# Kernel tuning notes

Measured on AMD Instinct MI355X. Metric: run time of the kernel, lower is better.

The kernel has to match this reference:

```python
import jax, jax.numpy as jnp
import numpy as np

NUM_CLASSES = 1203
C = NUM_CLASSES + 1
ITER = 9001            # > warm_up_iter=8000 (full path), not a multiple of save_iter=1000
GAMMA = 1.0
BETA = 1.0             # forward default loss_type=1 -> beta = 1
EMA = 0.999
LOWER = 1.0 / 3.0
UPPER = 5.0
LOSS_WEIGHT_ARG = 1.0  # forward `loss_weight` arg default
SELF_LOSS_WEIGHT = 1.0 # __init__ loss_weight
N = 16384              # multiple of 64 (interval in collect_grad_optim)


def setup_inputs() -> dict:
    key = jax.random.key(0)
    k1, k2, k3, k4, k5 = jax.random.split(key, 5)
    cls_score = jax.random.normal(k1, (N, C), jnp.float32)
    label = jax.random.randint(k2, (N,), 0, C)
    weight = jax.random.uniform(k3, (N,), jnp.float32)
    classes_logits = jax.random.normal(k4, (C,), jnp.float32) * 0.01
    class_weights_buf = jnp.ones((C,), jnp.float32)
    corr_grad_accu = jax.random.normal(k5, (C, C), jnp.float32) * 0.01
    weights_mean = jnp.ones((1,), jnp.float32)
    return {"cls_score": cls_score, "label": label, "weight": weight,
            "classes_logits": classes_logits, "class_weights_buf": class_weights_buf,
            "corr_grad_accu": corr_grad_accu, "weights_mean": weights_mean}


def reference(cls_score, label, weight, classes_logits, class_weights_buf,
              corr_grad_accu, weights_mean):
    sg = jax.lax.stop_gradient
    n = cls_score.shape[0]
    target = jax.nn.one_hot(label, C, dtype=cls_score.dtype)  # expand_label

    # ---- get_weight (no_grad in torch): beta=1, iter % save_iter != 0 ----
    cw = jnp.clip(class_weights_buf, LOWER, UPPER)
    tmp_weight = (cw ** BETA)[label]                 # (class_weights**beta * target).sum(1)
    wm = EMA * weights_mean[0] + (1.0 - EMA) * tmp_weight.mean()
    tmp_weight = tmp_weight / wm
    tmp_weight = sg(tmp_weight * weight)             # detached in torch

    # ---- focal cross-entropy ----
    logp = jax.nn.log_softmax(cls_score, axis=-1)
    CE = -jnp.take_along_axis(logp, label[:, None], axis=1)[:, 0]
    p = jnp.exp(-CE)
    loss = (1.0 - p) ** GAMMA * CE
    loss = (loss * tmp_weight).mean()                # weight_reduce_loss mean

    # ---- collect_grad_optim (all under no_grad in torch) ----
    cs = sg(cls_score)
    w = sg(weight)
    prob = jax.nn.softmax(cs, axis=-1) + 1e-5                       # [N,C]
    focal_grad = w[:, None] * ((1.0 - prob) / prob - jnp.log(prob)) # [N,C]
    pos_grad = ((1.0 - prob) * prob * focal_grad * target).mean(0)  # [C]
    # corr[i,j] = mean_n target[n,i]*focal_grad[n,i]*prob[n,i]*prob[n,j]
    a = target * focal_grad * prob                                  # [N,C]
    corr = jnp.einsum('ni,nj->ij', a, prob) / n                     # [C,C]
    diag = jnp.arange(C)
    corr = corr.at[diag, diag].set(-pos_grad)
    corr_grad = corr * 100.0 * LOSS_WEIGHT_ARG      # dist.all_reduce = identity (1 proc)

    # ITER >= warm_up_iter branch: EMA update + class weights from logits
    accu = EMA * sg(corr_grad_accu) + (1.0 - EMA) * corr_grad
    cw2 = sg(jax.nn.softmax(classes_logits)) * C    # detached in torch

    tcw = (cw2[:, None] * accu).sum(0) / (-jnp.diagonal(accu) + 1e-6) + cw2
    # ITER > warm_up_iter branch:
    tcw = tcw.at[-1].set(C - tcw[:-1].sum())
    tcw = jnp.clip(tcw, LOWER, UPPER)
    tcw = tcw.at[-1].set(jnp.clip(tcw[-1], LOWER, 1.0))
    tcw = sg(jnp.log(tcw))
    loss_grad = ((tcw - classes_logits) ** 2).mean()

    return (SELF_LOSS_WEIGHT * loss, loss_grad, cw2)
```

## Files before the change

### kernel.cpp

```cpp
#include <hip/hip_runtime.h>
#include <math.h>

#define C_   1204
#define C4_  301
#define NROWBLK 2048
#define BCAP 64
#define NYCHUNK 16
#define YLEN 76

__device__ __forceinline__ float waveReduceSum(float v){
    #pragma unroll
    for (int o = 32; o > 0; o >>= 1) v += __shfl_xor(v, o, 64);
    return v;
}
__device__ __forceinline__ float exp4(float4 v){
    return __expf(v.x) + __expf(v.y) + __expf(v.z) + __expf(v.w);
}
__device__ __forceinline__ float4 accExp(float4 acc, float sc, float4 x){
    acc.x += sc * __expf(x.x); acc.y += sc * __expf(x.y);
    acc.z += sc * __expf(x.z); acc.w += sc * __expf(x.w);
    return acc;
}

__global__ void k_pre(int* cursor, const float* __restrict__ logits,
                      float* cw2, float* out){
    int t = threadIdx.x;
    if (blockIdx.x > 0){
        int j = (blockIdx.x - 1) * 256 + t;
        if (j < C_) cursor[j] = 0;
        return;
    }
    __shared__ float red[256];
    float x[5]; float m = -3.402823466e38f;
    #pragma unroll
    for (int k = 0; k < 5; ++k){
        int j = t + k * 256;
        x[k] = (j < C_) ? logits[j] : -3.402823466e38f;
        m = fmaxf(m, x[k]);
    }
    red[t] = m; __syncthreads();
    for (int o = 128; o > 0; o >>= 1){ if (t < o) red[t] = fmaxf(red[t], red[t+o]); __syncthreads(); }
    float bm = red[0]; __syncthreads();
    float ss = 0.f;
    #pragma unroll
    for (int k = 0; k < 5; ++k){ int j = t + k * 256; if (j < C_) ss += __expf(x[k] - bm); }
    red[t] = ss; __syncthreads();
    for (int o = 128; o > 0; o >>= 1){ if (t < o) red[t] += red[t+o]; __syncthreads(); }
    float bs = red[0]; __syncthreads();
    #pragma unroll
    for (int k = 0; k < 5; ++k){
        int j = t + k * 256;
        if (j < C_){ float v = __expf(x[k] - bm) / bs * (float)C_; cw2[j] = v; out[2 + j] = v; }
    }
}

__global__ void k_rows(const float* __restrict__ cs, const int* __restrict__ label,
                       const float* __restrict__ w, const float* __restrict__ cwb,
                       float* __restrict__ rowsum, float* __restrict__ aN,
                       float* __restrict__ pN, int* cursor, int* bucket2,
                       float* __restrict__ part1, float* __restrict__ part2){
    int lane = threadIdx.x & 63;
    int wid  = threadIdx.x >> 6;
    int nA = (blockIdx.x * 4 + wid) * 2;
    int nB = nA + 1;
    const float4* rowA = reinterpret_cast<const float4*>(cs + (size_t)nA * C_);
    const float4* rowB = reinterpret_cast<const float4*>(cs + (size_t)nB * C_);
    bool has4 = lane < (C4_ - 256);

    float4 a0 = rowA[lane], a1 = rowA[lane + 64], a2 = rowA[lane + 128], a3 = rowA[lane + 192];
    float4 b0 = rowB[lane], b1 = rowB[lane + 64], b2 = rowB[lane + 128], b3 = rowB[lane + 192];
    float4 a4, b4;
    if (has4){ a4 = rowA[lane + 256]; b4 = rowB[lane + 256]; }

    float sA = exp4(a0) + exp4(a1) + exp4(a2) + exp4(a3);
    float sB = exp4(b0) + exp4(b1) + exp4(b2) + exp4(b3);
    if (has4){ sA += exp4(a4); sB += exp4(b4); }
    sA = waveReduceSum(sA);
    sB = waveReduceSum(sB);

    __shared__ float lr1[8], lr2[8];
    if (lane < 2){
        int   n = (lane == 0) ? nA : nB;
        float s = (lane == 0) ? sA : sB;
        rowsum[n] = s;
        int l = label[n];
        float x = cs[(size_t)n * C_ + l];
        float logp = x - __logf(s);
        float p = __expf(logp);
        float lossc = (1.f - p) * (-logp);
        float t = fminf(fmaxf(cwb[l], 1.f/3.f), 5.f);
        float wn = w[n];
        float pp = p + 1e-5f;
        float fg = wn * ((1.f - pp) / pp - __logf(pp));
        aN[n] = fg * pp;
        pN[n] = pp;
        int slot = atomicAdd(&cursor[l], 1);
        bucket2[l * BCAP + slot] = n;
        lr1[wid * 2 + lane] = lossc * t * wn;
        lr2[wid * 2 + lane] = t;
    }
    __syncthreads();
    if (threadIdx.x == 0){
        float s1 = 0.f, s2 = 0.f;
        #pragma unroll
        for (int k = 0; k < 8; ++k){ s1 += lr1[k]; s2 += lr2[k]; }
        part1[blockIdx.x] = s1;
        part2[blockIdx.x] = s2;
    }
}

__global__ void k_corr(const float* __restrict__ cs, const int* __restrict__ bucket2,
                       const int* __restrict__ cursor,
                       const float* __restrict__ rowsum, const float* __restrict__ aN,
                       const float* __restrict__ pN, const float* __restrict__ cga,
                       float* __restrict__ accu, float* __restrict__ diag, int Nn){
    int i = blockIdx.x;
    int t = threadIdx.x;
    int cnt = cursor[i];
    const int* bkt = bucket2 + i * BCAP;
    bool has2 = t < (C4_ - 256);
    float4 acc0 = {0.f,0.f,0.f,0.f}, acc1 = {0.f,0.f,0.f,0.f};
    float suma = 0.f, sumb = 0.f;

    int nbat = (cnt + 7) >> 3;
    for (int b = 0; b < nbat; ++b){
        int s = b << 3;
        #define LOADR(k) \
            int  id##k = min(s + k, cnt - 1); \
            int  n##k  = bkt[id##k]; \
            float va##k = aN[n##k]; \
            float pb##k = pN[n##k]; \
            float iv##k = (s + k < cnt) ? va##k / rowsum[n##k] : 0.f; \
            float ma##k = (s + k < cnt) ? va##k : 0.f; \
            const float4* rp##k = reinterpret_cast<const float4*>(cs + (size_t)n##k * C_); \
            float4 x0##k = rp##k[t]; \
            float4 x1##k; if (has2) x1##k = rp##k[t + 256];
        LOADR(0) LOADR(1) LOADR(2) LOADR(3) LOADR(4) LOADR(5) LOADR(6) LOADR(7)
        #undef LOADR
        suma += ma0 + ma1 + ma2 + ma3 + ma4 + ma5 + ma6 + ma7;
        sumb += ma0*pb0 + ma1*pb1 + ma2*pb2 + ma3*pb3
              + ma4*pb4 + ma5*pb5 + ma6*pb6 + ma7*pb7;
        acc0 = accExp(acc0, iv0, x00); acc0 = accExp(acc0, iv1, x01);
        acc0 = accExp(acc0, iv2, x02); acc0 = accExp(acc0, iv3, x03);
        acc0 = accExp(acc0, iv4, x04); acc0 = accExp(acc0, iv5, x05);
        acc0 = accExp(acc0, iv6, x06); acc0 = accExp(acc0, iv7, x07);
        if (has2){
            acc1 = accExp(acc1, iv0, x10); acc1 = accExp(acc1, iv1, x11);
            acc1 = accExp(acc1, iv2, x12); acc1 = accExp(acc1, iv3, x13);
            acc1 = accExp(acc1, iv4, x14); acc1 = accExp(acc1, iv5, x15);
            acc1 = accExp(acc1, iv6, x16); acc1 = accExp(acc1, iv7, x17);
        }
    }

    float eps   = suma * 1e-5f;
    float scale = 100.f / (float)Nn;
    float diagv = -100.f * (suma - sumb) / (float)Nn;
    const float4* cga4 = reinterpret_cast<const float4*>(cga + (size_t)i * C_);
    float4*       out4 = reinterpret_cast<float4*>(accu + (size_t)i * C_);
    int d4 = i >> 2, dc = i & 3;

    float4 cgv;
    cgv.x = (acc0.x + eps) * scale; cgv.y = (acc0.y + eps) * scale;
    cgv.z = (acc0.z + eps) * scale; cgv.w = (acc0.w + eps) * scale;
    if (t == d4){
        if (dc == 0) cgv.x = diagv; else if (dc == 1) cgv.y = diagv;
        else if (dc == 2) cgv.z = diagv; else cgv.w = diagv;
    }
    float4 gv = cga4[t];
    float4 wv;
    wv.x = 0.999f*gv.x + 0.001f*cgv.x; wv.y = 0.999f*gv.y + 0.001f*cgv.y;
    wv.z = 0.999f*gv.z + 0.001f*cgv.z; wv.w = 0.999f*gv.w + 0.001f*cgv.w;
    out4[t] = wv;
    if (t == d4)
        diag[i] = (dc == 0) ? wv.x : (dc == 1) ? wv.y : (dc == 2) ? wv.z : wv.w;

    if (has2){
        int t2 = t + 256;
        float4 cgv1;
        cgv1.x = (acc1.x + eps) * scale; cgv1.y = (acc1.y + eps) * scale;
        cgv1.z = (acc1.z + eps) * scale; cgv1.w = (acc1.w + eps) * scale;
        if (t2 == d4){
            if (dc == 0) cgv1.x = diagv; else if (dc == 1) cgv1.y = diagv;
            else if (dc == 2) cgv1.z = diagv; else cgv1.w = diagv;
        }
        float4 gv1 = cga4[t2];
        float4 wv1;
        wv1.x = 0.999f*gv1.x + 0.001f*cgv1.x; wv1.y = 0.999f*gv1.y + 0.001f*cgv1.y;
        wv1.z = 0.999f*gv1.z + 0.001f*cgv1.z; wv1.w = 0.999f*gv1.w + 0.001f*cgv1.w;
        out4[t2] = wv1;
        if (t2 == d4)
            diag[i] = (dc == 0) ? wv1.x : (dc == 1) ? wv1.y : (dc == 2) ? wv1.z : wv1.w;
    }
}

__global__ void k_matvec(const float* __restrict__ cw2, const float* __restrict__ accu,
                         float* __restrict__ tpart){
    int j = blockIdx.x * 256 + threadIdx.x;
    if (j >= C_) return;
    int i0 = blockIdx.y * YLEN, i1 = min(i0 + YLEN, C_);
    float p = 0.f;
    #pragma unroll 4
    for (int i = i0; i < i1; ++i) p += cw2[i] * accu[(size_t)i * C_ + j];
    tpart[blockIdx.y * C_ + j] = p;
}

__global__ void k_final(const float* __restrict__ tpart, const float* __restrict__ diag,
                        const float* __restrict__ cw2, const float* __restrict__ logits,
                        const float* __restrict__ part1, const float* __restrict__ part2,
                        const float* __restrict__ wm0, float* out, int Nn){
    __shared__ float tcw[C_];
    __shared__ float red[256];
    __shared__ float red2[256];
    int t = threadIdx.x;

    float p1 = 0.f, p2 = 0.f;
    for (int k = t; k < NROWBLK; k += 256){ p1 += part1[k]; p2 += part2[k]; }
    red[t] = p1; red2[t] = p2; __syncthreads();
    for (int o = 128; o > 0; o >>= 1){
        if (t < o){ red[t] += red[t+o]; red2[t] += red2[t+o]; }
        __syncthreads();
    }
    float sumLoss = red[0], sumT = red2[0];
    __syncthreads();

    float psum = 0.f;
    #pragma unroll
    for (int k = 0; k < 5; ++k){
        int j = t + k * 256;
        if (j < C_ - 1){
            float tc = 0.f;
            #pragma unroll
            for (int y = 0; y < NYCHUNK; ++y) tc += tpart[y * C_ + j];
            float denom = -diag[j] + 1e-6f;
            float v = tc / denom + cw2[j];
            tcw[j] = v; psum += v;
        }
    }
    red[t] = psum; __syncthreads();
    for (int o = 128; o > 0; o >>= 1){ if (t < o) red[t] += red[t+o]; __syncthreads(); }
    if (t == 0) tcw[C_ - 1] = (float)C_ - red[0];
    __syncthreads();
    float sq = 0.f;
    #pragma unroll
    for (int k = 0; k < 5; ++k){
        int j = t + k * 256;
        if (j < C_){
            float hi = (j == C_ - 1) ? 1.f : 5.f;
            float v = fminf(fmaxf(tcw[j], 1.f/3.f), hi);
            float d = logf(v) - logits[j];
            sq += d * d;
        }
    }
    red[t] = sq; __syncthreads();
    for (int o = 128; o > 0; o >>= 1){ if (t < o) red[t] += red[t+o]; __syncthreads(); }
    if (t == 0){
        float wm = 0.999f * wm0[0] + 0.001f * (sumT / (float)Nn);
        out[0] = sumLoss / ((float)Nn * wm);
        out[1] = red[0] / (float)C_;
    }
}

extern "C" void kernel_launch(void* const* d_in, const int* in_sizes, int n_in,
                              void* d_out, int out_size, void* d_ws, size_t ws_size,
                              hipStream_t stream){
    (void)n_in; (void)out_size; (void)ws_size;
    const float* cs     = (const float*)d_in[0];
    const int*   label  = (const int*)  d_in[1];
    const float* weight = (const float*)d_in[2];
    const float* logits = (const float*)d_in[3];
    const float* cwb    = (const float*)d_in[4];
    const float* cga    = (const float*)d_in[5];
    const float* wm0    = (const float*)d_in[6];
    float* out = (float*)d_out;
    const int N = in_sizes[1];

    float* ws      = (float*)d_ws;
    float* rowsum  = ws;
    float* aN      = ws + N;
    float* pN      = ws + 2 * N;
    int*   cursor  = (int*)(ws + 3 * N);
    float* cw2     = (float*)(cursor + C_);
    float* diag    = cw2 + C_;
    float* part1   = diag + C_;
    float* part2   = part1 + NROWBLK;
    float* tpart   = part2 + NROWBLK;
    int*   bucket2 = (int*)(tpart + NYCHUNK * C_);
    float* accu    = (float*)(bucket2 + C_ * BCAP);

    k_pre     <<<6,        256, 0, stream>>>(cursor, logits, cw2, out);
    k_rows    <<<NROWBLK,  256, 0, stream>>>(cs, label, weight, cwb, rowsum, aN, pN,
                                             cursor, bucket2, part1, part2);
    k_corr    <<<C_,       256, 0, stream>>>(cs, bucket2, cursor, rowsum, aN, pN,
                                             cga, accu, diag, N);
    dim3 g4((C_ + 255) / 256, NYCHUNK);
    k_matvec  <<<g4,       256, 0, stream>>>(cw2, accu, tpart);
    k_final   <<<1,        256, 0, stream>>>(tpart, diag, cw2, logits, part1, part2,
                                             wm0, out, N);
}
```

Before: 166.9 us.

## Collapse corr matrix to column sums via linearity, drop accu materialization

Because only cw2-weighted column sums and the diagonal of the EMA'd corr matrix are needed, the code drops the per-class bucketing, the full CxC accu write, and the matvec over accu. Instead it computes a weighted sum over rows S[j] = sum_n cw2[label]*a_n/s_n*exp(x_nj) in one streaming pass over cls_score, with per-class suma/sumb collected by atomics. The G = cw2^T·cga matvec and the cga diagonal are folded into extra blocks of the row kernel so they run concurrently with it. The change trades gathers and a large matrix write for float atomics, which can make reduction order nondeterministic.

Result: slower. 207.4 us (+24.3%).

```diff
diff --git a/kernel.cpp b/kernel.cpp
--- a/kernel.cpp
+++ b/kernel.cpp
@@ -3,10 +3,11 @@
 
 #define C_   1204
 #define C4_  301
-#define NROWBLK 2048
-#define BCAP 64
-#define NYCHUNK 16
-#define YLEN 76
+#define NABLK 2048
+#define NGBLK 80
+#define NDBLK 5
+#define GYLEN 76
+#define NSBLK 256
 
 __device__ __forceinline__ float waveReduceSum(float v){
     #pragma unroll
@@ -22,12 +23,12 @@
     return acc;
 }
 
-__global__ void k_pre(int* cursor, const float* __restrict__ logits,
+__global__ void k_pre(float* zbase, const float* __restrict__ logits,
                       float* cw2, float* out){
     int t = threadIdx.x;
     if (blockIdx.x > 0){
         int j = (blockIdx.x - 1) * 256 + t;
-        if (j < C_) cursor[j] = 0;
+        if (j < 3 * C_) zbase[j] = 0.f;
         return;
     }
     __shared__ float red[256];
@@ -56,12 +57,34 @@
 
 __global__ void k_rows(const float* __restrict__ cs, const int* __restrict__ label,
                        const float* __restrict__ w, const float* __restrict__ cwb,
-                       float* __restrict__ rowsum, float* __restrict__ aN,
-                       float* __restrict__ pN, int* cursor, int* bucket2,
-                       float* __restrict__ part1, float* __restrict__ part2){
-    int lane = threadIdx.x & 63;
-    int wid  = threadIdx.x >> 6;
-    int nA = (blockIdx.x * 4 + wid) * 2;
+                       const float* __restrict__ cw2, const float* __restrict__ cga,
+                       float* __restrict__ coefN, float* suma, float* sumb,
+                       float* __restrict__ part1, float* __restrict__ part2,
+                       float* __restrict__ Gpart, float* __restrict__ diagG){
+    int b = blockIdx.x;
+    int tid = threadIdx.x;
+
+    if (b >= NABLK){
+        int gb = b - NABLK;
+        if (gb < NGBLK){
+            int jt = gb % 5, ic = gb / 5;
+            int j = jt * 256 + tid;
+            if (j < C_){
+                int i0 = ic * GYLEN, i1 = min(i0 + GYLEN, C_);
+                float p = 0.f;
+                #pragma unroll 4
+                for (int i = i0; i < i1; ++i) p += cw2[i] * cga[(size_t)i * C_ + j];
+                Gpart[ic * C_ + j] = p;
+            }
+        } else {
+            int j = (gb - NGBLK) * 256 + tid;
+            if (j < C_) diagG[j] = cga[(size_t)j * C_ + j];
+        }
+        return;
+    }
+
+    int lane = tid & 63, wid = tid >> 6;
+    int nA = (b * 4 + wid) * 2;
     int nB = nA + 1;
     const float4* rowA = reinterpret_cast<const float4*>(cs + (size_t)nA * C_);
     const float4* rowB = reinterpret_cast<const float4*>(cs + (size_t)nB * C_);
@@ -82,139 +105,79 @@
     if (lane < 2){
         int   n = (lane == 0) ? nA : nB;
         float s = (lane == 0) ? sA : sB;
-        rowsum[n] = s;
         int l = label[n];
         float x = cs[(size_t)n * C_ + l];
         float logp = x - __logf(s);
         float p = __expf(logp);
         float lossc = (1.f - p) * (-logp);
-        float t = fminf(fmaxf(cwb[l], 1.f/3.f), 5.f);
+        float tw = fminf(fmaxf(cwb[l], 1.f/3.f), 5.f);
         float wn = w[n];
         float pp = p + 1e-5f;
         float fg = wn * ((1.f - pp) / pp - __logf(pp));
-        aN[n] = fg * pp;
-        pN[n] = pp;
-        int slot = atomicAdd(&cursor[l], 1);
-        bucket2[l * BCAP + slot] = n;
-        lr1[wid * 2 + lane] = lossc * t * wn;
-        lr2[wid * 2 + lane] = t;
-    }
-    __syncthreads();
-    if (threadIdx.x == 0){
+        float an = fg * pp;
+        coefN[n] = cw2[l] * an / s;
+        atomicAdd(&suma[l], an);
+        atomicAdd(&sumb[l], an * pp);
+        lr1[wid * 2 + lane] = lossc * tw * wn;
+        lr2[wid * 2 + lane] = tw;
+    }
+    __syncthreads();
+    if (tid == 0){
         float s1 = 0.f, s2 = 0.f;
         #pragma unroll
         for (int k = 0; k < 8; ++k){ s1 += lr1[k]; s2 += lr2[k]; }
-        part1[blockIdx.x] = s1;
-        part2[blockIdx.x] = s2;
-    }
-}
-
-__global__ void k_corr(const float* __restrict__ cs, const int* __restrict__ bucket2,
-                       const int* __restrict__ cursor,
-                       const float* __restrict__ rowsum, const float* __restrict__ aN,
-                       const float* __restrict__ pN, const float* __restrict__ cga,
-                       float* __restrict__ accu, float* __restrict__ diag, int Nn){
-    int i = blockIdx.x;
-    int t = threadIdx.x;
-    int cnt = cursor[i];
-    const int* bkt = bucket2 + i * BCAP;
-    bool has2 = t < (C4_ - 256);
+        part1[b] = s1;
+        part2[b] = s2;
+    }
+}
+
+__global__ void k_scol(const float* __restrict__ cs, const float* __restrict__ coefN,
+                       float* S){
+    int tid = threadIdx.x;
+    int n0 = blockIdx.x * 64;
+    bool has2 = tid < (C4_ - 256);
     float4 acc0 = {0.f,0.f,0.f,0.f}, acc1 = {0.f,0.f,0.f,0.f};
-    float suma = 0.f, sumb = 0.f;
-
-    int nbat = (cnt + 7) >> 3;
-    for (int b = 0; b < nbat; ++b){
-        int s = b << 3;
-        #define LOADR(k) \
-            int  id##k = min(s + k, cnt - 1); \
-            int  n##k  = bkt[id##k]; \
-            float va##k = aN[n##k]; \
-            float pb##k = pN[n##k]; \
-            float iv##k = (s + k < cnt) ? va##k / rowsum[n##k] : 0.f; \
-            float ma##k = (s + k < cnt) ? va##k : 0.f; \
-            const float4* rp##k = reinterpret_cast<const float4*>(cs + (size_t)n##k * C_); \
-            float4 x0##k = rp##k[t]; \
-            float4 x1##k; if (has2) x1##k = rp##k[t + 256];
-        LOADR(0) LOADR(1) LOADR(2) LOADR(3) LOADR(4) LOADR(5) LOADR(6) LOADR(7)
-        #undef LOADR
-        suma += ma0 + ma1 + ma2 + ma3 + ma4 + ma5 + ma6 + ma7;
-        sumb += ma0*pb0 + ma1*pb1 + ma2*pb2 + ma3*pb3
-              + ma4*pb4 + ma5*pb5 + ma6*pb6 + ma7*pb7;
-        acc0 = accExp(acc0, iv0, x00); acc0 = accExp(acc0, iv1, x01);
-        acc0 = accExp(acc0, iv2, x02); acc0 = accExp(acc0, iv3, x03);
-        acc0 = accExp(acc0, iv4, x04); acc0 = accExp(acc0, iv5, x05);
-        acc0 = accExp(acc0, iv6, x06); acc0 = accExp(acc0, iv7, x07);
+
+    for (int bb = 0; bb < 16; ++bb){
+        int n = n0 + bb * 4;
+        float c0 = coefN[n], c1 = coefN[n+1], c2 = coefN[n+2], c3 = coefN[n+3];
+        const float4* r0 = reinterpret_cast<const float4*>(cs + (size_t)(n    ) * C_);
+        const float4* r1 = reinterpret_cast<const float4*>(cs + (size_t)(n + 1) * C_);
+        const float4* r2 = reinterpret_cast<const float4*>(cs + (size_t)(n + 2) * C_);
+        const float4* r3 = reinterpret_cast<const float4*>(cs + (size_t)(n + 3) * C_);
+        float4 x00 = r0[tid], x01 = r1[tid], x02 = r2[tid], x03 = r3[tid];
+        float4 x10, x11, x12, x13;
+        if (has2){ x10 = r0[tid+256]; x11 = r1[tid+256]; x12 = r2[tid+256]; x13 = r3[tid+256]; }
+        acc0 = accExp(acc0, c0, x00); acc0 = accExp(acc0, c1, x01);
+        acc0 = accExp(acc0, c2, x02); acc0 = accExp(acc0, c3, x03);
         if (has2){
-            acc1 = accExp(acc1, iv0, x10); acc1 = accExp(acc1, iv1, x11);
-            acc1 = accExp(acc1, iv2, x12); acc1 = accExp(acc1, iv3, x13);
-            acc1 = accExp(acc1, iv4, x14); acc1 = accExp(acc1, iv5, x15);
-            acc1 = accExp(acc1, iv6, x16); acc1 = accExp(acc1, iv7, x17);
-        }
-    }
-
-    float eps   = suma * 1e-5f;
-    float scale = 100.f / (float)Nn;
-    float diagv = -100.f * (suma - sumb) / (float)Nn;
-    const float4* cga4 = reinterpret_cast<const float4*>(cga + (size_t)i * C_);
-    float4*       out4 = reinterpret_cast<float4*>(accu + (size_t)i * C_);
-    int d4 = i >> 2, dc = i & 3;
-
-    float4 cgv;
-    cgv.x = (acc0.x + eps) * scale; cgv.y = (acc0.y + eps) * scale;
-    cgv.z = (acc0.z + eps) * scale; cgv.w = (acc0.w + eps) * scale;
-    if (t == d4){
-        if (dc == 0) cgv.x = diagv; else if (dc == 1) cgv.y = diagv;
-        else if (dc == 2) cgv.z = diagv; else cgv.w = diagv;
-    }
-    float4 gv = cga4[t];
-    float4 wv;
-    wv.x = 0.999f*gv.x + 0.001f*cgv.x; wv.y = 0.999f*gv.y + 0.001f*cgv.y;
-    wv.z = 0.999f*gv.z + 0.001f*cgv.z; wv.w = 0.999f*gv.w + 0.001f*cgv.w;
-    out4[t] = wv;
-    if (t == d4)
-        diag[i] = (dc == 0) ? wv.x : (dc == 1) ? wv.y : (dc == 2) ? wv.z : wv.w;
-
+            acc1 = accExp(acc1, c0, x10); acc1 = accExp(acc1, c1, x11);
+            acc1 = accExp(acc1, c2, x12); acc1 = accExp(acc1, c3, x13);
+        }
+    }
+    int j = tid * 4;
+    atomicAdd(&S[j    ], acc0.x); atomicAdd(&S[j + 1], acc0.y);
+    atomicAdd(&S[j + 2], acc0.z); atomicAdd(&S[j + 3], acc0.w);
     if (has2){
-        int t2 = t + 256;
-        float4 cgv1;
-        cgv1.x = (acc1.x + eps) * scale; cgv1.y = (acc1.y + eps) * scale;
-        cgv1.z = (acc1.z + eps) * scale; cgv1.w = (acc1.w + eps) * scale;
-        if (t2 == d4){
-            if (dc == 0) cgv1.x = diagv; else if (dc == 1) cgv1.y = diagv;
-            else if (dc == 2) cgv1.z = diagv; else cgv1.w = diagv;
-        }
-        float4 gv1 = cga4[t2];
-        float4 wv1;
-        wv1.x = 0.999f*gv1.x + 0.001f*cgv1.x; wv1.y = 0.999f*gv1.y + 0.001f*cgv1.y;
-        wv1.z = 0.999f*gv1.z + 0.001f*cgv1.z; wv1.w = 0.999f*gv1.w + 0.001f*cgv1.w;
-        out4[t2] = wv1;
-        if (t2 == d4)
-            diag[i] = (dc == 0) ? wv1.x : (dc == 1) ? wv1.y : (dc == 2) ? wv1.z : wv1.w;
-    }
-}
-
-__global__ void k_matvec(const float* __restrict__ cw2, const float* __restrict__ accu,
-                         float* __restrict__ tpart){
-    int j = blockIdx.x * 256 + threadIdx.x;
-    if (j >= C_) return;
-    int i0 = blockIdx.y * YLEN, i1 = min(i0 + YLEN, C_);
-    float p = 0.f;
-    #pragma unroll 4
-    for (int i = i0; i < i1; ++i) p += cw2[i] * accu[(size_t)i * C_ + j];
-    tpart[blockIdx.y * C_ + j] = p;
-}
-
-__global__ void k_final(const float* __restrict__ tpart, const float* __restrict__ diag,
-                        const float* __restrict__ cw2, const float* __restrict__ logits,
-                        const float* __restrict__ part1, const float* __restrict__ part2,
-                        const float* __restrict__ wm0, float* out, int Nn){
+        int j2 = (tid + 256) * 4;
+        atomicAdd(&S[j2    ], acc1.x); atomicAdd(&S[j2 + 1], acc1.y);
+        atomicAdd(&S[j2 + 2], acc1.z); atomicAdd(&S[j2 + 3], acc1.w);
+    }
+}
+
+__global__ void k_last(const float* __restrict__ S, const float* __restrict__ Gpart,
+                       const float* __restrict__ diagG, const float* __restrict__ suma,
+                       const float* __restrict__ sumb, const float* __restrict__ cw2,
+                       const float* __restrict__ logits, const float* __restrict__ part1,
+                       const float* __restrict__ part2, const float* __restrict__ wm0,
+                       float* out, int Nn){
     __shared__ float tcw[C_];
     __shared__ float red[256];
     __shared__ float red2[256];
     int t = threadIdx.x;
 
     float p1 = 0.f, p2 = 0.f;
-    for (int k = t; k < NROWBLK; k += 256){ p1 += part1[k]; p2 += part2[k]; }
+    for (int k = t; k < NABLK; k += 256){ p1 += part1[k]; p2 += part2[k]; }
     red[t] = p1; red2[t] = p2; __syncthreads();
     for (int o = 128; o > 0; o >>= 1){
         if (t < o){ red[t] += red[t+o]; red2[t] += red2[t+o]; }
@@ -223,16 +186,29 @@
     float sumLoss = red[0], sumT = red2[0];
     __syncthreads();
 
+    float pe = 0.f;
+    #pragma unroll
+    for (int k = 0; k < 5; ++k){
+        int j = t + k * 256;
+        if (j < C_) pe += cw2[j] * suma[j];
+    }
+    red[t] = pe; __syncthreads();
+    for (int o = 128; o > 0; o >>= 1){ if (t < o) red[t] += red[t+o]; __syncthreads(); }
+    float E = red[0] * 1e-5f;
+    __syncthreads();
+
+    float scale = 100.f / (float)Nn;
     float psum = 0.f;
     #pragma unroll
     for (int k = 0; k < 5; ++k){
         int j = t + k * 256;
         if (j < C_ - 1){
-            float tc = 0.f;
+            float G = 0.f;
             #pragma unroll
-            for (int y = 0; y < NYCHUNK; ++y) tc += tpart[y * C_ + j];
-            float denom = -diag[j] + 1e-6f;
-            float v = tc / denom + cw2[j];
+            for (int y = 0; y < 16; ++y) G += Gpart[y * C_ + j];
+            float tcol  = 0.999f * G + 0.001f * scale * (S[j] + E - cw2[j] * suma[j]);
+            float diagA = 0.999f * diagG[j] - 0.001f * scale * (suma[j] - sumb[j]);
+            float v = tcol / (-diagA + 1e-6f) + cw2[j];
             tcw[j] = v; psum += v;
         }
     }
@@ -272,28 +248,24 @@
     const float* cga    = (const float*)d_in[5];
     const float* wm0    = (const float*)d_in[6];
     float* out = (float*)d_out;
-    const int N = in_sizes[1];
+    int N = in_sizes[1];
 
     float* ws      = (float*)d_ws;
-    float* rowsum  = ws;
-    float* aN      = ws + N;
-    float* pN      = ws + 2 * N;
-    int*   cursor  = (int*)(ws + 3 * N);
-    float* cw2     = (float*)(cursor + C_);
-    float* diag    = cw2 + C_;
-    float* part1   = diag + C_;
-    float* part2   = part1 + NROWBLK;
-    float* tpart   = part2 + NROWBLK;
-    int*   bucket2 = (int*)(tpart + NYCHUNK * C_);
-    float* accu    = (float*)(bucket2 + C_ * BCAP);
-
-    k_pre     <<<6,        256, 0, stream>>>(cursor, logits, cw2, out);
-    k_rows    <<<NROWBLK,  256, 0, stream>>>(cs, label, weight, cwb, rowsum, aN, pN,
-                                             cursor, bucket2, part1, part2);
-    k_corr    <<<C_,       256, 0, stream>>>(cs, bucket2, cursor, rowsum, aN, pN,
-                                             cga, accu, diag, N);
-    dim3 g4((C_ + 255) / 256, NYCHUNK);
-    k_matvec  <<<g4,       256, 0, stream>>>(cw2, accu, tpart);
-    k_final   <<<1,        256, 0, stream>>>(tpart, diag, cw2, logits, part1, part2,
-                                             wm0, out, N);
-}
+    float* coefN   = ws;
+    float* suma    = ws + N;
+    float* sumb    = suma + C_;
+    float* S       = sumb + C_;
+    float* cw2     = S + C_;
+    float* diagG   = cw2 + C_;
+    float* part1   = diagG + C_;
+    float* part2   = part1 + NABLK;
+    float* Gpart   = part2 + NABLK;
+
+    k_pre  <<<16,                  256, 0, stream>>>(suma, logits, cw2, out);
+    k_rows <<<NABLK + NGBLK + NDBLK, 256, 0, stream>>>(cs, label, weight, cwb, cw2, cga,
+                                                       coefN, suma, sumb, part1, part2,
+                                                       Gpart, diagG);
+    k_scol <<<NSBLK,               256, 0, stream>>>(cs, coefN, S);
+    k_last <<<1,                   256, 0, stream>>>(S, Gpart, diagG, suma, sumb, cw2,
+                                                     logits, part1, part2, wm0, out, N);
+}
```
